# Performance work log

Measured on AMD Instinct MI355X. Metric: run time of the kernel, lower is better.

The kernel has to match this reference:

```python
import jax, jax.numpy as jnp
import numpy as np

DIM, K, B, H, W = 64, 4, 16, 256, 256
KS, STRIDE, PAD = 5, 2, 1


def setup_inputs() -> dict:
    key = jax.random.key(0)
    ks = jax.random.split(key, 7)
    s = 0.05
    return {
        "x": jax.random.normal(ks[0], (B, DIM, H, W), jnp.float32),
        "fc1_w": jax.random.normal(ks[1], (K, DIM), jnp.float32) * s,
        "fc1_b": jnp.zeros((K,), jnp.float32),
        "fc2_w": jax.random.normal(ks[2], (K, K), jnp.float32) * s,
        "fc2_b": jnp.zeros((K,), jnp.float32),
        "weight": jax.random.normal(ks[3], (K, DIM, DIM, KS, KS), jnp.float32) * s,
        "bias": jax.random.normal(ks[4], (K, DIM), jnp.float32) * s,
    }


def reference(x, fc1_w, fc1_b, fc2_w, fc2_b, weight, bias):
    b, c, h, w = x.shape
    # --- KernelWeight attention: global avg pool -> 1x1 conv (linear) -> relu -> linear -> softmax
    pooled = x.mean(axis=(2, 3))                       # (B, C)
    a = jax.nn.relu(pooled @ fc1_w.T + fc1_b)          # (B, K)
    att = jax.nn.softmax(a @ fc2_w.T + fc2_b, axis=1)  # (B, K)
    # --- mix the K kernel bank per-sample
    agg_w = jnp.einsum('bk,koihw->boihw', att, weight)  # (B, Cout, Cin, ks, ks)
    agg_b = att @ bias                                  # (B, Cout)
    # --- per-sample conv (equivalent to torch grouped conv with groups=B)
    def conv_one(xi, wi, bi):
        y = jax.lax.conv_general_dilated(
            xi[None], wi,
            window_strides=(STRIDE, STRIDE),
            padding=[(PAD, PAD), (PAD, PAD)],
            dimension_numbers=('NCHW', 'OIHW', 'NCHW'))[0]
        return y + bi[:, None, None]
    out = jax.vmap(conv_one)(x, agg_w, agg_b)           # (B, Cout, Ho, Wo)
    bo, co, ho, wo = out.shape
    out = out.reshape(b, co, ho * wo)
    w_ret = agg_w.reshape(b * co, c, KS * KS).transpose(0, 2, 1)  # (B*Cout, ks*ks, Cin)
    return out, w_ret
```

## Files before the change

### kernel.cpp

```cpp
#include <hip/hip_runtime.h>
#include <math.h>

#define DIMC 64
#define KK 4
#define BATCH 16
#define HH 256
#define WW 256
#define HO 127
#define WO 127
#define PIX (HO*WO)
#define OUT_MAIN (BATCH*DIMC*PIX)

typedef __bf16 bf16x4 __attribute__((ext_vector_type(4)));
typedef __bf16 bf16x8 __attribute__((ext_vector_type(8)));
typedef float floatx16 __attribute__((ext_vector_type(16)));

#define BG_A2F    0
#define BG_XB     819200
#define BG_POOLED (BG_XB + 33554432)
#define BG_ATT    (BG_POOLED + 1024)
#define BG_AGGB   (BG_ATT + 64)
#define BG_END    (BG_AGGB + 1024)
#define BG_NEED_BYTES ((size_t)BG_END * 4)

#define SM_A2F    0
#define SM_POOLED 819200
#define SM_ATT    (SM_POOLED + 1024)
#define SM_AGGB   (SM_ATT + 64)

#define IXN 68
#define CIP 20

#define PROWS 8


__global__ void att_kernel(const float* __restrict__ fc1_w, const float* __restrict__ fc1_b,
                           const float* __restrict__ fc2_w, const float* __restrict__ fc2_b,
                           const float* __restrict__ bias,
                           const float* __restrict__ pooled_raw,
                           float* __restrict__ att_out, float* __restrict__ aggb_out) {
    __shared__ float satt[BATCH*KK];
    int tid = threadIdx.x;
    if (tid < BATCH) {
        int b = tid;
        const float* pooled = pooled_raw + b*DIMC;
        float a[KK];
        #pragma unroll
        for (int j = 0; j < KK; ++j) {
            float s = fc1_b[j];
            for (int i = 0; i < DIMC; ++i) s += pooled[i] * (1.f/65536.f) * fc1_w[j*DIMC + i];
            a[j] = fmaxf(s, 0.f);
        }
        float l[KK]; float m = -1e30f;
        #pragma unroll
        for (int j = 0; j < KK; ++j) {
            float s = fc2_b[j];
            #pragma unroll
            for (int k = 0; k < KK; ++k) s += a[k] * fc2_w[j*KK + k];
            l[j] = s; m = fmaxf(m, s);
        }
        float e[KK]; float Z = 0.f;
        #pragma unroll
        for (int j = 0; j < KK; ++j) { e[j] = expf(l[j] - m); Z += e[j]; }
        float invZ = 1.f / Z;
        #pragma unroll
        for (int j = 0; j < KK; ++j) {
            float av = e[j] * invZ;
            satt[b*KK + j] = av;
            att_out[b*KK + j] = av;
        }
    }
    __syncthreads();
    for (int idx = tid; idx < BATCH*DIMC; idx += blockDim.x) {
        int b = idx / DIMC, o = idx % DIMC;
        float s = 0.f;
        #pragma unroll
        for (int k = 0; k < KK; ++k) s += satt[b*KK + k] * bias[k*DIMC + o];
        aggb_out[idx] = s;
    }
}

__global__ void agg_kernel(const float* __restrict__ weight, const float* __restrict__ att,
                           __bf16* __restrict__ a2, float* __restrict__ wret) {
    int v = blockIdx.x * 256 + threadIdx.x;
    int i = v & 63;
    int t = (v >> 6) % 25;
    int o = (v / 1600) & 63;
    int b = v / 102400;
    float s = 0.f;
    #pragma unroll
    for (int k = 0; k < KK; ++k)
        s += att[b*KK + k] * weight[((k*DIMC + o)*DIMC + i)*25 + t];
    wret[v] = s;
    a2[(((b*4 + (i >> 4))*25 + t)*64 + o)*16 + (i & 15)] = (__bf16)s;
}


__global__ __launch_bounds__(256) void pool_cvt_kernel(const float* __restrict__ x,
                                                       __bf16* __restrict__ xb,
                                                       float* __restrict__ pooled) {
    int yg = blockIdx.x, ch = blockIdx.y, b = blockIdx.z;
    int tid = threadIdx.x;
    float acc[16];
    #pragma unroll
    for (int s = 0; s < 16; ++s) acc[s] = 0.f;
    const float* srcbase = x + (((size_t)(b*DIMC + ch*16))*HH + yg*PROWS)*WW + tid;
    __bf16* dstbase = xb + ((((size_t)(b*4 + ch))*HH + yg*PROWS)*WW + tid)*16;
    for (int ry = 0; ry < PROWS; ++ry) {
        const float* src = srcbase + (size_t)ry*WW;
        float v[16];
        #pragma unroll
        for (int s = 0; s < 16; ++s) v[s] = src[(size_t)s*HH*WW];
        bf16x8 lo, hi;
        #pragma unroll
        for (int j = 0; j < 8; ++j) { lo[j] = (__bf16)v[j]; hi[j] = (__bf16)v[j+8]; }
        __bf16* dst = dstbase + (size_t)ry*WW*16;
        *(bf16x8*)dst = lo;
        *(bf16x8*)(dst + 8) = hi;
        #pragma unroll
        for (int s = 0; s < 16; ++s) acc[s] += v[s];
    }
    #pragma unroll
    for (int s = 0; s < 16; ++s) {
        float t = acc[s];
        for (int off = 32; off > 0; off >>= 1) t += __shfl_down(t, off, 64);
        acc[s] = t;
    }
    __shared__ float part[4][16];
    int lane = tid & 63, w = tid >> 6;
    if (lane == 0) {
        #pragma unroll
        for (int s = 0; s < 16; ++s) part[w][s] = acc[s];
    }
    __syncthreads();
    if (tid < 16) {
        float p = part[0][tid] + part[1][tid] + part[2][tid] + part[3][tid];
        atomicAdd(&pooled[b*DIMC + ch*16 + tid], p);
    }
}

__global__ __launch_bounds__(128) void conv_big_kernel(const __bf16* __restrict__ xb,
                                                       const __bf16* __restrict__ a2,
                                                       const float* __restrict__ aggb,
                                                       float* __restrict__ out) {
    __shared__ __bf16 lin[11*IXN*CIP];
    int ct = blockIdx.x;
    int rg = blockIdx.y;
    int b  = blockIdx.z;
    int tid = threadIdx.x, lane = tid & 63, rp = tid >> 6;
    int n = lane & 31, h = lane >> 5;
    int gx0 = ct*64 - 1, gy0 = rg*8 - 1;
    int bconst = 40*n + 8*h;
    floatx16 acc00 = {}, acc01 = {}, acc10 = {}, acc11 = {};

    for (int c = 0; c < 4; ++c) {
        __syncthreads();
        const __bf16* xsrc = xb + ((size_t)(b*4 + c))*HH*WW*16;
        #pragma unroll
        for (int it = 0; it < 12; ++it) {
            int idx = it*128 + tid;
            if (idx < 1474) {
                int r = idx / 134;
                int q = idx - r*134;
                int ix = q >> 1, hh = q & 1;
                int gy = gy0 + r, gx = gx0 + ix;
                bf16x8 vv = {};
                if ((unsigned)gy < (unsigned)HH && (unsigned)gx < (unsigned)WW)
                    vv = *(const bf16x8*)(xsrc + ((size_t)gy*WW + gx)*16 + hh*8);
                __bf16* dp = lin + (r*IXN + ix)*CIP + hh*8;
                bf16x4 vlo = {vv[0], vv[1], vv[2], vv[3]};
                bf16x4 vhi = {vv[4], vv[5], vv[6], vv[7]};
                *(bf16x4*)dp = vlo;
                *(bf16x4*)(dp + 4) = vhi;
            }
        }
        __syncthreads();

        const __bf16* ap = a2 + ((size_t)(b*4 + c)*25*64 + n)*16 + h*8;
        #pragma unroll 5
        for (int t = 0; t < 25; ++t) {
            int dy = t / 5, dx = t - dy*5;
            bf16x8 a0 = *(const bf16x8*)(ap + t*1024);
            bf16x8 a1 = *(const bf16x8*)(ap + t*1024 + 512);
            {
                int iy = 4*rp + dy;
                const __bf16* bp = lin + (iy*IXN + dx)*CIP + bconst;
                bf16x4 l0 = *(const bf16x4*)bp;
                bf16x4 h0 = *(const bf16x4*)(bp + 4);
                bf16x8 bb = __builtin_shufflevector(l0, h0, 0,1,2,3,4,5,6,7);
                acc00 = __builtin_amdgcn_mfma_f32_32x32x16_bf16(a0, bb, acc00, 0, 0, 0);
                acc01 = __builtin_amdgcn_mfma_f32_32x32x16_bf16(a1, bb, acc01, 0, 0, 0);
            }
            {
                int iy = 4*rp + 2 + dy;
                const __bf16* bp = lin + (iy*IXN + dx)*CIP + bconst;
                bf16x4 l0 = *(const bf16x4*)bp;
                bf16x4 h0 = *(const bf16x4*)(bp + 4);
                bf16x8 bb = __builtin_shufflevector(l0, h0, 0,1,2,3,4,5,6,7);
                acc10 = __builtin_amdgcn_mfma_f32_32x32x16_bf16(a0, bb, acc10, 0, 0, 0);
                acc11 = __builtin_amdgcn_mfma_f32_32x32x16_bf16(a1, bb, acc11, 0, 0, 0);
            }
        }
    }

    int oxg = ct*32 + n;
    if (oxg < WO) {
        #pragma unroll
        for (int nt = 0; nt < 2; ++nt) {
            int oy = rg*4 + 2*rp + nt;
            if (oy >= HO) continue;
            #pragma unroll
            for (int mh = 0; mh < 2; ++mh) {
                const floatx16& acc = nt ? (mh ? acc11 : acc10) : (mh ? acc01 : acc00);
                #pragma unroll
                for (int reg = 0; reg < 16; ++reg) {
                    int cout = mh*32 + (reg & 3) + 8*(reg >> 2) + 4*h;
                    float val = acc[reg] + aggb[b*DIMC + cout];
                    out[(size_t)(b*DIMC + cout)*PIX + oy*WO + oxg] = val;
                }
            }
        }
    }
}


__global__ void pool_kernel(const float* __restrict__ x, float* __restrict__ pooled) {
    int plane = blockIdx.x >> 1, half = blockIdx.x & 1;
    const float4* p = (const float4*)(x + (size_t)plane * (HH*WW)) + half * 8192;
    float s = 0.f;
    for (int k = threadIdx.x; k < 8192; k += 256) {
        float4 v = p[k];
        s += (v.x + v.y) + (v.z + v.w);
    }
    for (int off = 32; off > 0; off >>= 1) s += __shfl_down(s, off, 64);
    __shared__ float red[4];
    if ((threadIdx.x & 63) == 0) red[threadIdx.x >> 6] = s;
    __syncthreads();
    if (threadIdx.x == 0) atomicAdd(&pooled[plane], red[0] + red[1] + red[2] + red[3]);
}

__global__ __launch_bounds__(256) void conv_small_kernel(const float* __restrict__ x,
                                                         const __bf16* __restrict__ a2,
                                                         const float* __restrict__ aggb,
                                                         float* __restrict__ out) {
    __shared__ __bf16 lin[11*IXN*CIP];
    int ct = blockIdx.x;
    int rg = blockIdx.y;
    int b  = blockIdx.z;
    int tid = threadIdx.x, lane = tid & 63, w = tid >> 6;
    int mh = w & 1;
    int rp = w >> 1;
    int n = lane & 31, h = lane >> 5;
    floatx16 acc0 = {}, acc1 = {};
    int gx0 = ct*64 - 1;
    int gy0 = rg*8 - 1;
    const float* xbse = x + (size_t)b * (DIMC*HH*WW);
    int bconst = 40*n + 8*h;

    for (int c = 0; c < 4; ++c) {
        __syncthreads();
        for (int rr = w; rr < 176; rr += 4) {
            int s = rr / 11, iy = rr - s*11;
            int gy = gy0 + iy;
            bool rowok = (unsigned)gy < (unsigned)HH;
            const float* row = xbse + (size_t)(c*16 + s)*(HH*WW) + gy*WW;
            int gx = gx0 + lane;
            float v0 = 0.f;
            if (rowok && (unsigned)gx < (unsigned)WW) v0 = row[gx];
            lin[(iy*IXN + lane)*CIP + s] = (__bf16)v0;
            int ix2 = lane + 64;
            if (ix2 < 67) {
                int gx2 = gx0 + ix2;
                float v1 = 0.f;
                if (rowok && (unsigned)gx2 < (unsigned)WW) v1 = row[gx2];
                lin[(iy*IXN + ix2)*CIP + s] = (__bf16)v1;
            }
        }
        __syncthreads();

        const __bf16* ap = a2 + ((size_t)(b*4 + c)*25*64 + (size_t)(mh*32 + n))*16 + h*8;
        #pragma unroll 5
        for (int t = 0; t < 25; ++t) {
            int dy = t / 5, dx = t - dy*5;
            bf16x8 a = *(const bf16x8*)(ap + t*1024);
            {
                int iy = 4*rp + dy;
                const __bf16* bp = lin + (iy*IXN + dx)*CIP + bconst;
                bf16x4 lo = *(const bf16x4*)bp;
                bf16x4 hi = *(const bf16x4*)(bp + 4);
                bf16x8 bb = __builtin_shufflevector(lo, hi, 0,1,2,3,4,5,6,7);
                acc0 = __builtin_amdgcn_mfma_f32_32x32x16_bf16(a, bb, acc0, 0, 0, 0);
            }
            {
                int iy = 4*rp + 2 + dy;
                const __bf16* bp = lin + (iy*IXN + dx)*CIP + bconst;
                bf16x4 lo = *(const bf16x4*)bp;
                bf16x4 hi = *(const bf16x4*)(bp + 4);
                bf16x8 bb = __builtin_shufflevector(lo, hi, 0,1,2,3,4,5,6,7);
                acc1 = __builtin_amdgcn_mfma_f32_32x32x16_bf16(a, bb, acc1, 0, 0, 0);
            }
        }
    }

    int oxg = ct*32 + n;
    if (oxg < WO) {
        #pragma unroll
        for (int nt = 0; nt < 2; ++nt) {
            int oy = rg*4 + 2*rp + nt;
            if (oy >= HO) continue;
            const floatx16& acc = nt ? acc1 : acc0;
            #pragma unroll
            for (int reg = 0; reg < 16; ++reg) {
                int row = (reg & 3) + 8*(reg >> 2) + 4*h;
                int cout = mh*32 + row;
                float val = acc[reg] + aggb[b*DIMC + cout];
                out[(size_t)(b*DIMC + cout)*PIX + oy*WO + oxg] = val;
            }
        }
    }
}

extern "C" void kernel_launch(void* const* d_in, const int* in_sizes, int n_in,
                              void* d_out, int out_size, void* d_ws, size_t ws_size,
                              hipStream_t stream) {
    const float* x      = (const float*)d_in[0];
    const float* fc1_w  = (const float*)d_in[1];
    const float* fc1_b  = (const float*)d_in[2];
    const float* fc2_w  = (const float*)d_in[3];
    const float* fc2_b  = (const float*)d_in[4];
    const float* weight = (const float*)d_in[5];
    const float* bias   = (const float*)d_in[6];
    float* out = (float*)d_out;
    float* ws  = (float*)d_ws;

    if (ws_size >= BG_NEED_BYTES) {
        __bf16* a2 = (__bf16*)(ws + BG_A2F);
        __bf16* xb = (__bf16*)(ws + BG_XB);
        hipMemsetAsync(ws + BG_POOLED, 0, 1024*sizeof(float), stream);
        pool_cvt_kernel<<<dim3(HH/PROWS, 4, BATCH), 256, 0, stream>>>(x, xb, ws + BG_POOLED);
        att_kernel<<<1, 256, 0, stream>>>(fc1_w, fc1_b, fc2_w, fc2_b, bias,
                                          ws + BG_POOLED, ws + BG_ATT, ws + BG_AGGB);
        agg_kernel<<<BATCH*DIMC*DIMC*25/256, 256, 0, stream>>>(weight, ws + BG_ATT,
                                                               a2, out + OUT_MAIN);
        conv_big_kernel<<<dim3(4, 32, BATCH), 128, 0, stream>>>(xb, a2, ws + BG_AGGB, out);
    } else {
        __bf16* a2 = (__bf16*)(ws + SM_A2F);
        hipMemsetAsync(ws + SM_POOLED, 0, 1024*sizeof(float), stream);
        pool_kernel<<<2*BATCH*DIMC, 256, 0, stream>>>(x, ws + SM_POOLED);
        att_kernel<<<1, 256, 0, stream>>>(fc1_w, fc1_b, fc2_w, fc2_b, bias,
                                          ws + SM_POOLED, ws + SM_ATT, ws + SM_AGGB);
        agg_kernel<<<BATCH*DIMC*DIMC*25/256, 256, 0, stream>>>(weight, ws + SM_ATT,
                                                               a2, out + OUT_MAIN);
        conv_small_kernel<<<dim3(4, 32, BATCH), 256, 0, stream>>>(x, a2, ws + SM_AGGB, out);
    }
}
```

Before: 578.6 us.

## Prefetch next channel tile into registers, vectorize pool-convert, parallelize attention fc1

The conv kernel now loads the next input-channel chunk from global memory into registers while MFMAs run on the current chunk held in LDS. This overlaps global load latency with compute at the cost of 12 extra bf16x8 registers per thread, which may reduce occupancy. The pool/convert kernel reads float4 per lane and handles 2 rows per wave instead of looping 8 rows per thread, giving wider loads. The attention fc1 step is split across 256 threads using shuffle reductions instead of running 16 serial threads.

```diff
diff --git a/kernel.cpp b/kernel.cpp
--- a/kernel.cpp
+++ b/kernel.cpp
@@ -13,6 +13,7 @@
 
 typedef __bf16 bf16x4 __attribute__((ext_vector_type(4)));
 typedef __bf16 bf16x8 __attribute__((ext_vector_type(8)));
+typedef float floatx4 __attribute__((ext_vector_type(4)));
 typedef float floatx16 __attribute__((ext_vector_type(16)));
 
 #define BG_A2F    0
@@ -39,24 +40,29 @@
                            const float* __restrict__ bias,
                            const float* __restrict__ pooled_raw,
                            float* __restrict__ att_out, float* __restrict__ aggb_out) {
+    __shared__ float sa[BATCH][KK];
     __shared__ float satt[BATCH*KK];
     int tid = threadIdx.x;
+    {
+        int b = tid >> 4, j = (tid >> 2) & 3, q = tid & 3;
+        const float* pooled = pooled_raw + b*DIMC + q*16;
+        const float* wrow   = fc1_w + j*DIMC + q*16;
+        float s = 0.f;
+        #pragma unroll
+        for (int i = 0; i < 16; ++i) s += pooled[i] * (1.f/65536.f) * wrow[i];
+        s += __shfl_xor(s, 1, 64);
+        s += __shfl_xor(s, 2, 64);
+        if (q == 0) sa[b][j] = fmaxf(s + fc1_b[j], 0.f);
+    }
+    __syncthreads();
     if (tid < BATCH) {
         int b = tid;
-        const float* pooled = pooled_raw + b*DIMC;
-        float a[KK];
-        #pragma unroll
-        for (int j = 0; j < KK; ++j) {
-            float s = fc1_b[j];
-            for (int i = 0; i < DIMC; ++i) s += pooled[i] * (1.f/65536.f) * fc1_w[j*DIMC + i];
-            a[j] = fmaxf(s, 0.f);
-        }
         float l[KK]; float m = -1e30f;
         #pragma unroll
         for (int j = 0; j < KK; ++j) {
             float s = fc2_b[j];
             #pragma unroll
-            for (int k = 0; k < KK; ++k) s += a[k] * fc2_w[j*KK + k];
+            for (int k = 0; k < KK; ++k) s += sa[b][k] * fc2_w[j*KK + k];
             l[j] = s; m = fmaxf(m, s);
         }
         float e[KK]; float Z = 0.f;
@@ -100,25 +106,32 @@
                                                        __bf16* __restrict__ xb,
                                                        float* __restrict__ pooled) {
     int yg = blockIdx.x, ch = blockIdx.y, b = blockIdx.z;
-    int tid = threadIdx.x;
+    int tid = threadIdx.x, lane = tid & 63, w = tid >> 6;
     float acc[16];
     #pragma unroll
     for (int s = 0; s < 16; ++s) acc[s] = 0.f;
-    const float* srcbase = x + (((size_t)(b*DIMC + ch*16))*HH + yg*PROWS)*WW + tid;
-    __bf16* dstbase = xb + ((((size_t)(b*4 + ch))*HH + yg*PROWS)*WW + tid)*16;
-    for (int ry = 0; ry < PROWS; ++ry) {
-        const float* src = srcbase + (size_t)ry*WW;
-        float v[16];
-        #pragma unroll
-        for (int s = 0; s < 16; ++s) v[s] = src[(size_t)s*HH*WW];
-        bf16x8 lo, hi;
-        #pragma unroll
-        for (int j = 0; j < 8; ++j) { lo[j] = (__bf16)v[j]; hi[j] = (__bf16)v[j+8]; }
-        __bf16* dst = dstbase + (size_t)ry*WW*16;
-        *(bf16x8*)dst = lo;
-        *(bf16x8*)(dst + 8) = hi;
-        #pragma unroll
-        for (int s = 0; s < 16; ++s) acc[s] += v[s];
+    #pragma unroll
+    for (int ry = 0; ry < 2; ++ry) {
+        int y = yg*PROWS + w*2 + ry;
+        const float* src = x + (((size_t)(b*DIMC + ch*16))*HH + y)*WW + lane*4;
+        floatx4 v[16];
+        #pragma unroll
+        for (int s = 0; s < 16; ++s) v[s] = *(const floatx4*)(src + (size_t)s*HH*WW);
+        __bf16* dst = xb + ((((size_t)(b*4 + ch))*HH + y)*WW + lane*4)*16;
+        #pragma unroll
+        for (int p = 0; p < 4; ++p) {
+            bf16x8 lo, hi;
+            #pragma unroll
+            for (int j = 0; j < 8; ++j) {
+                lo[j] = (__bf16)v[j][p];
+                hi[j] = (__bf16)v[j+8][p];
+            }
+            *(bf16x8*)(dst + p*16) = lo;
+            *(bf16x8*)(dst + p*16 + 8) = hi;
+        }
+        #pragma unroll
+        for (int s = 0; s < 16; ++s)
+            acc[s] += (v[s][0] + v[s][1]) + (v[s][2] + v[s][3]);
     }
     #pragma unroll
     for (int s = 0; s < 16; ++s) {
@@ -127,7 +140,6 @@
         acc[s] = t;
     }
     __shared__ float part[4][16];
-    int lane = tid & 63, w = tid >> 6;
     if (lane == 0) {
         #pragma unroll
         for (int s = 0; s < 16; ++s) part[w][s] = acc[s];
@@ -153,9 +165,27 @@
     int bconst = 40*n + 8*h;
     floatx16 acc00 = {}, acc01 = {}, acc10 = {}, acc11 = {};
 
+    bf16x8 pre[12];
+    {
+        const __bf16* xsrc = xb + ((size_t)(b*4 + 0))*HH*WW*16;
+        #pragma unroll
+        for (int it = 0; it < 12; ++it) {
+            int idx = it*128 + tid;
+            bf16x8 vv = {};
+            if (idx < 1474) {
+                int r = idx / 134;
+                int q = idx - r*134;
+                int ix = q >> 1, hh = q & 1;
+                int gy = gy0 + r, gx = gx0 + ix;
+                if ((unsigned)gy < (unsigned)HH && (unsigned)gx < (unsigned)WW)
+                    vv = *(const bf16x8*)(xsrc + ((size_t)gy*WW + gx)*16 + hh*8);
+            }
+            pre[it] = vv;
+        }
+    }
+
     for (int c = 0; c < 4; ++c) {
         __syncthreads();
-        const __bf16* xsrc = xb + ((size_t)(b*4 + c))*HH*WW*16;
         #pragma unroll
         for (int it = 0; it < 12; ++it) {
             int idx = it*128 + tid;
@@ -163,18 +193,31 @@
                 int r = idx / 134;
                 int q = idx - r*134;
                 int ix = q >> 1, hh = q & 1;
-                int gy = gy0 + r, gx = gx0 + ix;
-                bf16x8 vv = {};
-                if ((unsigned)gy < (unsigned)HH && (unsigned)gx < (unsigned)WW)
-                    vv = *(const bf16x8*)(xsrc + ((size_t)gy*WW + gx)*16 + hh*8);
                 __bf16* dp = lin + (r*IXN + ix)*CIP + hh*8;
-                bf16x4 vlo = {vv[0], vv[1], vv[2], vv[3]};
-                bf16x4 vhi = {vv[4], vv[5], vv[6], vv[7]};
+                bf16x4 vlo = {pre[it][0], pre[it][1], pre[it][2], pre[it][3]};
+                bf16x4 vhi = {pre[it][4], pre[it][5], pre[it][6], pre[it][7]};
                 *(bf16x4*)dp = vlo;
                 *(bf16x4*)(dp + 4) = vhi;
             }
         }
         __syncthreads();
+        if (c < 3) {
+            const __bf16* xsrc = xb + ((size_t)(b*4 + c + 1))*HH*WW*16;
+            #pragma unroll
+            for (int it = 0; it < 12; ++it) {
+                int idx = it*128 + tid;
+                bf16x8 vv = {};
+                if (idx < 1474) {
+                    int r = idx / 134;
+                    int q = idx - r*134;
+                    int ix = q >> 1, hh = q & 1;
+                    int gy = gy0 + r, gx = gx0 + ix;
+                    if ((unsigned)gy < (unsigned)HH && (unsigned)gx < (unsigned)WW)
+                        vv = *(const bf16x8*)(xsrc + ((size_t)gy*WW + gx)*16 + hh*8);
+                }
+                pre[it] = vv;
+            }
+        }
 
         const __bf16* ap = a2 + ((size_t)(b*4 + c)*25*64 + n)*16 + h*8;
         #pragma unroll 5
```

After: 564.2 us. 1.03x faster.
